# Kernel optimization log

Measured on AMD Instinct MI355X. Metric: run time of the kernel, lower is better.

Reference implementation:

```python
import jax, jax.numpy as jnp
import numpy as np

N = 20000      # nodes
E = 640000     # edges (avg degree 32)
IN = 32        # input_dim
HID = 256      # hidden_dim
H = 8          # num_heads
Dh = HID // H  # head_dim = 32
TD = 32        # time_dim
L = 3          # num_layers
OUT = 2


def setup_inputs() -> dict:
    key = jax.random.key(0)
    ks = jax.random.split(key, 20)
    def w(k, sh):
        return (jax.random.normal(k, sh, jnp.float32) * 0.05)
    return {
        "x": jax.random.normal(ks[0], (N, IN), jnp.float32),
        "timestamps": jax.random.uniform(ks[1], (N,), jnp.float32),
        "edge_index": jax.random.randint(ks[2], (2, E), 0, N, jnp.int32),
        "batch": jnp.zeros((N,), jnp.int32),
        "time_freq": jax.random.normal(ks[3], (TD // 2,), jnp.float32),
        "inW": w(ks[4], (IN, HID)), "inb": jnp.zeros((HID,), jnp.float32),
        "qW": w(ks[5], (L, HID + TD, HID)), "qb": jnp.zeros((L, HID), jnp.float32),
        "kW": w(ks[6], (L, HID + TD, HID)), "kb": jnp.zeros((L, HID), jnp.float32),
        "vW": w(ks[7], (L, HID, HID)), "vb": jnp.zeros((L, HID), jnp.float32),
        "oW": w(ks[8], (L, HID, HID)), "ob": jnp.zeros((L, HID), jnp.float32),
        "c1W": w(ks[9], (HID, HID // 2)), "c1b": jnp.zeros((HID // 2,), jnp.float32),
        "c2W": w(ks[10], (HID // 2, OUT)), "c2b": jnp.zeros((OUT,), jnp.float32),
    }


def reference(x, timestamps, time_freq, inW, inb, qW, qb, kW, kb, vW, vb,
              oW, ob, c1W, c1b, c2W, c2b, edge_index, batch):
    n = x.shape[0]
    src, dst = edge_index[0], edge_index[1]

    # Functional time encoding (node-level timestamps branch)
    t = (timestamps - timestamps.min()) / (timestamps.max() - timestamps.min() + 1e-8)
    wt = t[:, None] * time_freq[None, :]                      # [N, TD/2]
    tf = jnp.concatenate([jnp.cos(wt), jnp.sin(wt)], axis=-1)  # [N, TD]

    h = x @ inW + inb                                          # [N, HID]
    scale = 1.0 / np.sqrt(Dh).astype(np.float32)

    for l in range(L):
        xt = jnp.concatenate([h, tf], axis=-1)                 # [N, HID+TD]
        Q = (xt @ qW[l] + qb[l]).reshape(n, H, Dh)
        K = (xt @ kW[l] + kb[l]).reshape(n, H, Dh)
        V = (h @ vW[l] + vb[l]).reshape(n, H, Dh)

        # per-edge attention scores [E, H]
        scores = jnp.einsum('ehd,ehd->eh', Q[dst], K[src]) * scale

        # segment softmax over incoming edges of each dst node
        m = jax.ops.segment_max(scores, dst, num_segments=n)   # [N, H]
        e = jnp.exp(scores - m[dst])
        s = jax.ops.segment_sum(e, dst, num_segments=n)        # [N, H]
        att = e / s[dst]                                       # [E, H]

        msgs = att[..., None] * V[src]                         # [E, H, Dh]
        out = jax.ops.segment_sum(msgs, dst, num_segments=n)   # [N, H, Dh]
        out = out.reshape(n, HID) @ oW[l] + ob[l]
        h = jax.nn.elu(out)

    # global mean pool (single graph: batch all zeros)
    cnt = jax.ops.segment_sum(jnp.ones((n, 1), h.dtype), batch, num_segments=1)
    g = jax.ops.segment_sum(h, batch, num_segments=1) / jnp.maximum(cnt, 1.0)

    logits = jax.nn.relu(g @ c1W + c1b) @ c2W + c2b            # [1, OUT]
    return logits
```

## Files before the change

### kernel.cpp

```cpp
#include <hip/hip_runtime.h>
#include <math.h>

#define HID 256
#define TD 32
#define NL 3
#define C1DIM 128
#define OUTDIM 2
#define QKVW 768
#define KVSTRIDE 576

using half8  = __attribute__((ext_vector_type(8))) _Float16;
using half4v = __attribute__((ext_vector_type(4))) _Float16;
using half2v = __attribute__((ext_vector_type(2))) _Float16;
using f32x4  = __attribute__((ext_vector_type(4))) float;

typedef __attribute__((address_space(1))) void gbl_void_t;
typedef __attribute__((address_space(3))) void lds_void_t;

__device__ __forceinline__ void load16_to_lds(const void* g, void* l) {
  __builtin_amdgcn_global_load_lds((const gbl_void_t*)g, (lds_void_t*)l, 16, 0, 0);
}

__device__ __forceinline__ int sdot4i(unsigned a, unsigned b, int acc) {
#if __has_builtin(__builtin_amdgcn_sdot4)
  return __builtin_amdgcn_sdot4((int)a, (int)b, acc, false);
#else
#pragma unroll
  for (int i = 0; i < 4; ++i)
    acc += (int)(signed char)(a >> (8 * i)) * (int)(signed char)(b >> (8 * i));
  return acc;
#endif
}

__device__ __forceinline__ void i8x4_to_f32(unsigned w, float* o) {
  o[0] = (float)(int)(signed char)(w);
  o[1] = (float)(int)(signed char)(w >> 8);
  o[2] = (float)(int)(signed char)(w >> 16);
  o[3] = (float)(int)(signed char)(w >> 24);
}

__global__ __launch_bounds__(1024) void k_tsmm(const float* __restrict__ ts,
                                               float* __restrict__ mmf,
                                               int* __restrict__ deg, int n) {
  int t = threadIdx.x;
  float lmin = INFINITY, lmax = -INFINITY;
  for (int i = t; i < n; i += 1024) {
    float v = ts[i];
    lmin = fminf(lmin, v);
    lmax = fmaxf(lmax, v);
    deg[i] = 0;
  }
#pragma unroll
  for (int off = 32; off >= 1; off >>= 1) {
    lmin = fminf(lmin, __shfl_xor(lmin, off));
    lmax = fmaxf(lmax, __shfl_xor(lmax, off));
  }
  __shared__ float wmin[16], wmax[16];
  int lane = t & 63, w = t >> 6;
  if (lane == 0) { wmin[w] = lmin; wmax[w] = lmax; }
  __syncthreads();
  if (t == 0) {
    float a = INFINITY, b = -INFINITY;
    for (int i = 0; i < 16; ++i) { a = fminf(a, wmin[i]); b = fmaxf(b, wmax[i]); }
    mmf[0] = a; mmf[1] = b;
  }
}

__global__ void k_enc(const float* __restrict__ ts, const float* __restrict__ freq,
                      const float* __restrict__ mmf, const float* __restrict__ x,
                      _Float16* __restrict__ tfh, _Float16* __restrict__ xh, int n) {
  int idx = blockIdx.x * blockDim.x + threadIdx.x;
  int nt = n * TD;
  if (idx < nt) {
    int node = idx >> 5, j = idx & 31;
    float t = (ts[node] - mmf[0]) / (mmf[1] - mmf[0] + 1e-8f);
    float w = t * freq[j & 15];
    tfh[idx] = (_Float16)((j < 16) ? cosf(w) : sinf(w));
  } else if (idx < nt + n * 32) {
    int i2 = idx - nt;
    xh[i2] = (_Float16)x[i2];
  }
}

__global__ void k_prep(const float* __restrict__ inW, const float* __restrict__ qW,
                       const float* __restrict__ kW, const float* __restrict__ vW,
                       const float* __restrict__ oW, const float* __restrict__ qb,
                       const float* __restrict__ kb, const float* __restrict__ vb,
                       _Float16* __restrict__ inWt, _Float16* __restrict__ qkvWt,
                       float* __restrict__ qkvb, _Float16* __restrict__ oWt) {
  int idx = blockIdx.x * blockDim.x + threadIdx.x;
  const int S0 = 32 * HID;
  const int KQ = HID + TD;
  const int S1 = NL * QKVW * KQ;
  const int S2 = NL * QKVW;
  const int S3 = NL * HID * HID;
  if (idx < S0) {
    int nrow = idx / 32, k = idx - nrow * 32;
    inWt[idx] = (_Float16)inW[k * HID + nrow];
  } else if ((idx -= S0) < S1) {
    int l = idx / (QKVW * KQ);
    int rem = idx - l * (QKVW * KQ);
    int nrow = rem / KQ;
    int k = rem - nrow * KQ;
    float v;
    if (nrow < 256)      v = qW[(size_t)l * KQ * HID + (size_t)k * HID + nrow];
    else if (nrow < 512) v = kW[(size_t)l * KQ * HID + (size_t)k * HID + (nrow - 256)];
    else                 v = (k < HID) ? vW[(size_t)l * HID * HID + (size_t)k * HID + (nrow - 512)] : 0.f;
    qkvWt[idx] = (_Float16)v;
  } else if ((idx -= S1) < S2) {
    int l = idx / QKVW;
    int j = idx - l * QKVW;
    float v;
    if (j < 256)      v = qb[l * HID + j];
    else if (j < 512) v = kb[l * HID + (j - 256)];
    else              v = vb[l * HID + (j - 512)];
    qkvb[idx] = v;
  } else if ((idx -= S2) < S3) {
    int l = idx / (HID * HID);
    int rem = idx - l * (HID * HID);
    int nrow = rem / HID;
    int k = rem - nrow * HID;
    oWt[idx] = (_Float16)oW[(size_t)l * HID * HID + (size_t)k * HID + nrow];
  }
}

__global__ void k_count(const int* __restrict__ dst, int* deg, int e) {
  int i = blockIdx.x * blockDim.x + threadIdx.x;
  if (i < e) atomicAdd(&deg[dst[i]], 1);
}

__global__ __launch_bounds__(256) void k_scan_part(const int* __restrict__ deg,
                                                   int* __restrict__ bsum, int n) {
  int t = threadIdx.x;
  int idx = blockIdx.x * 256 + t;
  int v = (idx < n) ? deg[idx] : 0;
  int lane = t & 63, w = t >> 6;
  int x = v;
#pragma unroll
  for (int off = 1; off < 64; off <<= 1) {
    int y = __shfl_up(x, off);
    if (lane >= off) x += y;
  }
  __shared__ int ws[4];
  if (lane == 63) ws[w] = x;
  __syncthreads();
  if (t == 0) bsum[blockIdx.x] = ws[0] + ws[1] + ws[2] + ws[3];
}

__global__ __launch_bounds__(64) void k_scan_mid(const int* __restrict__ bsum,
                                                 int* __restrict__ boff, int nb) {
  int lane = threadIdx.x;
  int carry = 0;
  for (int base = 0; base < nb; base += 64) {
    int i = base + lane;
    int v = (i < nb) ? bsum[i] : 0;
    int x = v;
#pragma unroll
    for (int off = 1; off < 64; off <<= 1) {
      int y = __shfl_up(x, off);
      if (lane >= off) x += y;
    }
    if (i < nb) boff[i] = carry + x - v;
    carry += __shfl(x, 63);
  }
}

__global__ __launch_bounds__(256) void k_scan_apply(const int* __restrict__ deg,
                                                    const int* __restrict__ boff,
                                                    int* __restrict__ row_ptr,
                                                    int* __restrict__ cursor, int n, int e) {
  int t = threadIdx.x;
  int idx = blockIdx.x * 256 + t;
  int v = (idx < n) ? deg[idx] : 0;
  int lane = t & 63, w = t >> 6;
  int x = v;
#pragma unroll
  for (int off = 1; off < 64; off <<= 1) {
    int y = __shfl_up(x, off);
    if (lane >= off) x += y;
  }
  __shared__ int ws[4];
  if (lane == 63) ws[w] = x;
  __syncthreads();
  int wpre = 0;
  for (int i = 0; i < w; ++i) wpre += ws[i];
  if (idx < n) {
    row_ptr[idx] = boff[blockIdx.x] + wpre + x - v;
    cursor[idx] = 0;
  }
  if (idx == 0) row_ptr[n] = e;
}

__global__ void k_scatter(const int* __restrict__ src, const int* __restrict__ dst,
                          const int* __restrict__ row_ptr, int* cursor,
                          int* __restrict__ colbuf, int e) {
  int i = blockIdx.x * blockDim.x + threadIdx.x;
  if (i >= e) return;
  int d = dst[i];
  int p = atomicAdd(&cursor[d], 1);
  colbuf[row_ptr[d] + p] = src[i];
}

__global__ __launch_bounds__(256) void k_gemm_f16(
    const _Float16* __restrict__ A1, int K1,
    const _Float16* __restrict__ A2, int K2,
    const _Float16* __restrict__ Bt,
    const float* __restrict__ bias,
    _Float16* __restrict__ C,
    int M, int Ncols, int Ktot, int act) {
  __shared__ half8 smem8[2 * 768];
  char* smem = (char*)smem8;
  const int tid = threadIdx.x;
  const int lane = tid & 63, wave = tid >> 6;
  const int wm = wave >> 1, wn = wave & 1;
  const int row0 = blockIdx.y * 128;
  const int col0 = blockIdx.x * 64;

  auto stage = [&](int buf, int k0) {
    char* sA = smem + buf * 12288;
    char* sB = sA + 8192;
#pragma unroll
    for (int i = 0; i < 2; ++i) {
      int kg = i * 2 + (wave >> 1);
      int row = (wave & 1) * 64 + lane;
      int grow = row0 + row; if (grow > M - 1) grow = M - 1;
      int k = k0 + kg * 8;
      const _Float16* src = (k < K1) ? (A1 + (size_t)grow * K1 + k)
                                     : (A2 + (size_t)grow * K2 + (k - K1));
      load16_to_lds(src, sA + (i * 256 + wave * 64) * 16);
    }
    {
      const _Float16* src = Bt + (size_t)(col0 + lane) * Ktot + k0 + wave * 8;
      load16_to_lds(src, sB + wave * 64 * 16);
    }
  };

  f32x4 acc[4][2];
#pragma unroll
  for (int mf = 0; mf < 4; ++mf)
#pragma unroll
    for (int nf = 0; nf < 2; ++nf) acc[mf][nf] = f32x4{0.f, 0.f, 0.f, 0.f};

  const int nsteps = Ktot >> 5;
  int cur = 0;
  stage(0, 0);
  __syncthreads();
  for (int st = 0; st < nsteps; ++st) {
    if (st + 1 < nsteps) stage(cur ^ 1, (st + 1) * 32);
    char* sA = smem + cur * 12288;
    char* sB = sA + 8192;
    half8 af[4], bf[2];
#pragma unroll
    for (int mf = 0; mf < 4; ++mf) {
      int slot = (lane >> 4) * 128 + wm * 64 + mf * 16 + (lane & 15);
      af[mf] = *(const half8*)(sA + slot * 16);
    }
#pragma unroll
    for (int nf = 0; nf < 2; ++nf) {
      int slot = (lane >> 4) * 64 + wn * 32 + nf * 16 + (lane & 15);
      bf[nf] = *(const half8*)(sB + slot * 16);
    }
#pragma unroll
    for (int mf = 0; mf < 4; ++mf)
#pragma unroll
      for (int nf = 0; nf < 2; ++nf)
        acc[mf][nf] = __builtin_amdgcn_mfma_f32_16x16x32_f16(af[mf], bf[nf], acc[mf][nf], 0, 0, 0);
    __syncthreads();
    cur ^= 1;
  }

  const int rbase = row0 + wm * 64 + (lane >> 4) * 4;
  const int cbase = col0 + wn * 32 + (lane & 15);
#pragma unroll
  for (int nf = 0; nf < 2; ++nf) {
    int col = cbase + nf * 16;
    float bv = bias[col];
#pragma unroll
    for (int mf = 0; mf < 4; ++mf) {
#pragma unroll
      for (int r = 0; r < 4; ++r) {
        int row = rbase + mf * 16 + r;
        if (row < M) {
          float v = acc[mf][nf][r] + bv;
          if (act == 1) v = (v > 0.f) ? v : expm1f(v);
          C[(size_t)row * Ncols + col] = (_Float16)v;
        }
      }
    }
  }
}

__global__ __launch_bounds__(256) void k_cvt8(const _Float16* __restrict__ QKV,
                                              unsigned char* __restrict__ KV8, int n) {
  int node = blockIdx.x * 8 + (threadIdx.x >> 5);
  if (node >= n) return;
  int t32 = threadIdx.x & 31;
  const _Float16* base = QKV + (size_t)node * QKVW + t32 * 8;
  half8 kh = *(const half8*)(base + 256);
  half8 vh = *(const half8*)(base + 512);
  float kf[8], vf[8];
  float kmax = 0.f, vmax = 0.f;
#pragma unroll
  for (int j = 0; j < 8; ++j) {
    kf[j] = (float)kh[j]; kmax = fmaxf(kmax, fabsf(kf[j]));
    vf[j] = (float)vh[j]; vmax = fmaxf(vmax, fabsf(vf[j]));
  }
  kmax = fmaxf(kmax, __shfl_xor(kmax, 1)); kmax = fmaxf(kmax, __shfl_xor(kmax, 2));
  vmax = fmaxf(vmax, __shfl_xor(vmax, 1)); vmax = fmaxf(vmax, __shfl_xor(vmax, 2));
  float kinv = (kmax > 0.f) ? (127.f / kmax) : 0.f;
  float vinv = (vmax > 0.f) ? (127.f / vmax) : 0.f;
  unsigned kp0 = 0, kp1 = 0, vp0 = 0, vp1 = 0;
#pragma unroll
  for (int j = 0; j < 4; ++j) {
    kp0 |= ((unsigned)((int)rintf(kf[j] * kinv)) & 255u) << (8 * j);
    kp1 |= ((unsigned)((int)rintf(kf[j + 4] * kinv)) & 255u) << (8 * j);
    vp0 |= ((unsigned)((int)rintf(vf[j] * vinv)) & 255u) << (8 * j);
    vp1 |= ((unsigned)((int)rintf(vf[j + 4] * vinv)) & 255u) << (8 * j);
  }
  unsigned char* out = KV8 + (size_t)node * KVSTRIDE;
  *(uint2*)(out + t32 * 8) = uint2{kp0, kp1};
  *(uint2*)(out + 256 + t32 * 8) = uint2{vp0, vp1};
  if ((t32 & 3) == 0) {
    half2v sp;
    sp.x = (_Float16)(kmax * (1.f / 127.f));
    sp.y = (_Float16)(vmax * (1.f / 127.f));
    *(half2v*)(out + 512 + (t32 >> 2) * 4) = sp;
  }
}

__global__ __launch_bounds__(256) void k_attn(const _Float16* __restrict__ QKV,
                                              const unsigned char* __restrict__ KV8,
                                              const int* __restrict__ row_ptr,
                                              const int* __restrict__ colbuf,
                                              _Float16* __restrict__ out, int n) {
  __shared__ float sm_m[4][8], sm_s[4][8];
  __shared__ float sm_a[4][32][9];
  int tid = threadIdx.x;
  int g = tid >> 5, t32 = tid & 31;
  int nl = g >> 1, hf = g & 1;
  int node = blockIdx.x * 4 + nl;
  bool act = node < n;
  int beg = 0, end = 0;
  if (act) { beg = row_ptr[node]; end = row_ptr[node + 1]; }
  int mid = beg + ((end - beg + 1) >> 1);
  int lo = hf ? mid : beg;
  int hi = hf ? end : mid;
  int d = t32 * 8;
  const float scale = 0.17677669529663687f;

  float qf[8] = {0.f, 0.f, 0.f, 0.f, 0.f, 0.f, 0.f, 0.f};
  if (act) {
    half8 qh = *(const half8*)(QKV + (size_t)node * QKVW + d);
#pragma unroll
    for (int j = 0; j < 8; ++j) qf[j] = (float)qh[j] * scale;
  }
  float qmax = 0.f;
#pragma unroll
  for (int j = 0; j < 8; ++j) qmax = fmaxf(qmax, fabsf(qf[j]));
  qmax = fmaxf(qmax, __shfl_xor(qmax, 1));
  qmax = fmaxf(qmax, __shfl_xor(qmax, 2));
  float qinv = (qmax > 0.f) ? (127.f / qmax) : 0.f;
  float sq = qmax * (1.f / 127.f);
  unsigned q8x = 0, q8y = 0;
#pragma unroll
  for (int j = 0; j < 4; ++j) {
    q8x |= ((unsigned)((int)rintf(qf[j] * qinv)) & 255u) << (8 * j);
    q8y |= ((unsigned)((int)rintf(qf[j + 4] * qinv)) & 255u) << (8 * j);
  }

  float m = -INFINITY, s = 0.f;
  float a[8] = {0.f, 0.f, 0.f, 0.f, 0.f, 0.f, 0.f, 0.f};
  int scoff = 512 + (t32 >> 2) * 4;

  for (int i = lo; i < hi; i += 4) {
    uint2 kb[4], vb[4];
    float skj[4], svj[4];
#pragma unroll
    for (int j = 0; j < 4; ++j) {
      int ii = i + j; if (ii > hi - 1) ii = hi - 1;
      int sn = colbuf[ii];
      const unsigned char* b = KV8 + (size_t)sn * KVSTRIDE;
      kb[j] = *(const uint2*)(b + t32 * 8);
      vb[j] = *(const uint2*)(b + 256 + t32 * 8);
      unsigned scw = *(const unsigned*)(b + scoff);
      union { unsigned u; half2v h; } sc; sc.u = scw;
      skj[j] = (float)sc.h.x;
      svj[j] = (float)sc.h.y;
    }
    float p[4];
#pragma unroll
    for (int j = 0; j < 4; ++j) {
      int idot = sdot4i(kb[j].x, q8x, 0);
      idot = sdot4i(kb[j].y, q8y, idot);
      p[j] = (float)idot;
    }
#pragma unroll
    for (int j = 0; j < 4; ++j) {
      p[j] += __shfl_xor(p[j], 1);
      p[j] += __shfl_xor(p[j], 2);
      p[j] *= sq * skj[j];
      if (i + j >= hi) p[j] = -INFINITY;
    }
#pragma unroll
    for (int j = 0; j < 4; ++j) {
      float vf[8];
      i8x4_to_f32(vb[j].x, vf);
      i8x4_to_f32(vb[j].y, vf + 4);
      float sc_ = p[j];
      if (sc_ <= m) {
        float e2 = __expf(sc_ - m);
        s += e2;
        float ev = e2 * svj[j];
#pragma unroll
        for (int q = 0; q < 8; ++q) a[q] = fmaf(ev, vf[q], a[q]);
      } else {
        float f = __expf(m - sc_);
        s = s * f + 1.f;
#pragma unroll
        for (int q = 0; q < 8; ++q) a[q] = fmaf(a[q], f, svj[j] * vf[q]);
        m = sc_;
      }
    }
  }

  if (hf == 1 && act) {
    if ((t32 & 3) == 0) { sm_m[nl][t32 >> 2] = m; sm_s[nl][t32 >> 2] = s; }
#pragma unroll
    for (int q = 0; q < 8; ++q) sm_a[nl][t32][q] = a[q];
  }
  __syncthreads();
  if (hf == 0 && act) {
    float m1 = sm_m[nl][t32 >> 2], s1 = sm_s[nl][t32 >> 2];
    float M = fmaxf(m, m1);
    float f0 = (s > 0.f) ? __expf(m - M) : 0.f;
    float f1 = (s1 > 0.f) ? __expf(m1 - M) : 0.f;
    float S = s * f0 + s1 * f1;
    float inv = (S > 0.f) ? (1.f / S) : 0.f;
    half8 o;
#pragma unroll
    for (int q = 0; q < 8; ++q) o[q] = (_Float16)((a[q] * f0 + sm_a[nl][t32][q] * f1) * inv);
    *(half8*)(out + (size_t)node * HID + d) = o;
  }
}

__global__ __launch_bounds__(256) void k_pool_partial(const _Float16* __restrict__ h,
                                                      float* __restrict__ partial, int n) {
  int b = blockIdx.x, t = threadIdx.x;
  float s = 0.f;
  for (int r = b; r < n; r += 256) s += (float)h[(size_t)r * HID + t];
  partial[b * HID + t] = s;
}

__global__ __launch_bounds__(256) void k_final(const float* __restrict__ partial,
                                               const float* __restrict__ c1W,
                                               const float* __restrict__ c1b,
                                               const float* __restrict__ c2W,
                                               const float* __restrict__ c2b,
                                               float* __restrict__ out, int n) {
  __shared__ float gl[HID];
  __shared__ float r1[C1DIM];
  int t = threadIdx.x;
  float s = 0.f;
  for (int b = 0; b < 256; b++) s += partial[b * HID + t];
  gl[t] = s / (float)n;
  __syncthreads();
  if (t < C1DIM) {
    float a = c1b[t];
    for (int k = 0; k < HID; k++) a += gl[k] * c1W[k * C1DIM + t];
    r1[t] = fmaxf(a, 0.f);
  }
  __syncthreads();
  if (t < OUTDIM) {
    float a = c2b[t];
    for (int k = 0; k < C1DIM; k++) a += r1[k] * c2W[k * OUTDIM + t];
    out[t] = a;
  }
}

extern "C" void kernel_launch(void* const* d_in, const int* in_sizes, int n_in,
                              void* d_out, int out_size, void* d_ws, size_t ws_size,
                              hipStream_t stream) {
  const float* x    = (const float*)d_in[0];
  const float* ts   = (const float*)d_in[1];
  const int*   ei   = (const int*)d_in[2];
  const float* freq = (const float*)d_in[4];
  const float* inW  = (const float*)d_in[5];
  const float* inb  = (const float*)d_in[6];
  const float* qW   = (const float*)d_in[7];
  const float* qb   = (const float*)d_in[8];
  const float* kW   = (const float*)d_in[9];
  const float* kb   = (const float*)d_in[10];
  const float* vW   = (const float*)d_in[11];
  const float* vb   = (const float*)d_in[12];
  const float* oW   = (const float*)d_in[13];
  const float* ob   = (const float*)d_in[14];
  const float* c1W  = (const float*)d_in[15];
  const float* c1b  = (const float*)d_in[16];
  const float* c2W  = (const float*)d_in[17];
  const float* c2b  = (const float*)d_in[18];

  int n = in_sizes[1];
  int e = in_sizes[2] / 2;
  const int* src = ei;
  const int* dst = ei + e;
  int nb = (n + 255) / 256;

  char* w = (char*)d_ws;
  size_t off = 0;
  auto alloc = [&](size_t bytes) -> char* {
    char* p = w + off;
    off = (off + bytes + 255) & ~(size_t)255;
    return p;
  };
  _Float16* tfh     = (_Float16*)alloc((size_t)n * TD * 2);
  _Float16* xh      = (_Float16*)alloc((size_t)n * 32 * 2);
  _Float16* h       = (_Float16*)alloc((size_t)n * HID * 2);
  _Float16* QKV     = (_Float16*)alloc((size_t)n * QKVW * 2);
  unsigned char* KV8 = (unsigned char*)alloc((size_t)n * KVSTRIDE);
  _Float16* ao      = (_Float16*)alloc((size_t)n * HID * 2);
  _Float16* inWt    = (_Float16*)alloc((size_t)32 * HID * 2);
  _Float16* qkvWt   = (_Float16*)alloc((size_t)NL * QKVW * (HID + TD) * 2);
  float*    qkvb    = (float*)alloc((size_t)NL * QKVW * 4);
  _Float16* oWt     = (_Float16*)alloc((size_t)NL * HID * HID * 2);
  int*      deg     = (int*)alloc((size_t)n * 4);
  int*      cursor  = (int*)alloc((size_t)n * 4);
  int*      row_ptr = (int*)alloc((size_t)(n + 1) * 4);
  int*      colbuf  = (int*)alloc((size_t)e * 4);
  int*      bsum    = (int*)alloc((size_t)nb * 4);
  int*      boff    = (int*)alloc((size_t)nb * 4);
  float*    partial = (float*)alloc((size_t)256 * HID * 4);
  float*    mmf     = (float*)alloc(256);

  int b256 = 256;
  hipLaunchKernelGGL(k_tsmm, dim3(1), dim3(1024), 0, stream, ts, mmf, deg, n);
  hipLaunchKernelGGL(k_enc, dim3((n * 64 + 255) / 256), dim3(b256), 0, stream,
                     ts, freq, mmf, x, tfh, xh, n);
  {
    int total = 32 * HID + NL * QKVW * (HID + TD) + NL * QKVW + NL * HID * HID;
    hipLaunchKernelGGL(k_prep, dim3((total + 255) / 256), dim3(b256), 0, stream,
                       inW, qW, kW, vW, oW, qb, kb, vb, inWt, qkvWt, qkvb, oWt);
  }
  hipLaunchKernelGGL(k_count, dim3((e + 255) / 256), dim3(b256), 0, stream, dst, deg, e);
  hipLaunchKernelGGL(k_scan_part, dim3(nb), dim3(b256), 0, stream, deg, bsum, n);
  hipLaunchKernelGGL(k_scan_mid, dim3(1), dim3(64), 0, stream, bsum, boff, nb);
  hipLaunchKernelGGL(k_scan_apply, dim3(nb), dim3(b256), 0, stream, deg, boff, row_ptr, cursor, n, e);
  hipLaunchKernelGGL(k_scatter, dim3((e + 255) / 256), dim3(b256), 0, stream, src, dst, row_ptr, cursor, colbuf, e);

  dim3 ggrid_h(HID / 64, (n + 127) / 128);
  dim3 ggrid_qkv(QKVW / 64, (n + 127) / 128);
  hipLaunchKernelGGL(k_gemm_f16, ggrid_h, dim3(b256), 0, stream,
                     xh, 32, xh, 32, inWt, inb, h, n, HID, 32, 0);

  for (int l = 0; l < NL; ++l) {
    const _Float16* qkvWtl = qkvWt + (size_t)l * QKVW * (HID + TD);
    const float*    qkvbl  = qkvb + (size_t)l * QKVW;
    const _Float16* oWtl   = oWt + (size_t)l * HID * HID;
    hipLaunchKernelGGL(k_gemm_f16, ggrid_qkv, dim3(b256), 0, stream,
                       h, HID, tfh, TD, qkvWtl, qkvbl, QKV, n, QKVW, HID + TD, 0);
    hipLaunchKernelGGL(k_cvt8, dim3((n + 7) / 8), dim3(b256), 0, stream,
                       QKV, KV8, n);
    hipLaunchKernelGGL(k_attn, dim3((n + 3) / 4), dim3(b256), 0, stream,
                       QKV, KV8, row_ptr, colbuf, ao, n);
    hipLaunchKernelGGL(k_gemm_f16, ggrid_h, dim3(b256), 0, stream,
                       ao, HID, ao, HID, oWtl, ob + l * HID, h, n, HID, HID, 1);
  }

  hipLaunchKernelGGL(k_pool_partial, dim3(256), dim3(b256), 0, stream, h, partial, n);
  hipLaunchKernelGGL(k_final, dim3(1), dim3(b256), 0, stream, partial, c1W, c1b, c2W, c2b, (float*)d_out, n);
}
```

Baseline: 480.4 us.

## Store int8 K/V head-major and assign one 8-lane group per node-head in attention

The quantized K/V buffer changes from node-major to head-major: each head of each node gets a 64-byte row with K and V bytes interleaved, and the per-head scales move to a separate array. The attention kernel now has each block handle one head for 32 nodes, with 8 lanes per node-head walking the whole edge list. This removes the two-way edge split and its shared-memory merge, and keeps each block's gathers inside one head's slice so they stay local in cache. In exchange, each node's edge list is processed serially per head, so nodes with many edges run longer with no split to spread the work, and the dot-product reduction needs an extra shuffle step.

```diff
diff --git a/kernel.cpp b/kernel.cpp
--- a/kernel.cpp
+++ b/kernel.cpp
@@ -7,7 +7,6 @@
 #define C1DIM 128
 #define OUTDIM 2
 #define QKVW 768
-#define KVSTRIDE 576
 
 using half8  = __attribute__((ext_vector_type(8))) _Float16;
 using half4v = __attribute__((ext_vector_type(4))) _Float16;
@@ -30,13 +29,6 @@
     acc += (int)(signed char)(a >> (8 * i)) * (int)(signed char)(b >> (8 * i));
   return acc;
 #endif
-}
-
-__device__ __forceinline__ void i8x4_to_f32(unsigned w, float* o) {
-  o[0] = (float)(int)(signed char)(w);
-  o[1] = (float)(int)(signed char)(w >> 8);
-  o[2] = (float)(int)(signed char)(w >> 16);
-  o[3] = (float)(int)(signed char)(w >> 24);
 }
 
 __global__ __launch_bounds__(1024) void k_tsmm(const float* __restrict__ ts,
@@ -291,10 +283,12 @@
 }
 
 __global__ __launch_bounds__(256) void k_cvt8(const _Float16* __restrict__ QKV,
-                                              unsigned char* __restrict__ KV8, int n) {
+                                              unsigned char* __restrict__ KV8,
+                                              half2v* __restrict__ SC, int n) {
   int node = blockIdx.x * 8 + (threadIdx.x >> 5);
   if (node >= n) return;
   int t32 = threadIdx.x & 31;
+  int h = t32 >> 2, p = t32 & 3;
   const _Float16* base = QKV + (size_t)node * QKVW + t32 * 8;
   half8 kh = *(const half8*)(base + 256);
   half8 vh = *(const half8*)(base + 512);
@@ -317,130 +311,104 @@
     vp0 |= ((unsigned)((int)rintf(vf[j] * vinv)) & 255u) << (8 * j);
     vp1 |= ((unsigned)((int)rintf(vf[j + 4] * vinv)) & 255u) << (8 * j);
   }
-  unsigned char* out = KV8 + (size_t)node * KVSTRIDE;
-  *(uint2*)(out + t32 * 8) = uint2{kp0, kp1};
-  *(uint2*)(out + 256 + t32 * 8) = uint2{vp0, vp1};
-  if ((t32 & 3) == 0) {
+  unsigned char* out = KV8 + (((size_t)h * n + node) << 6);
+  *(uint2*)(out + (2 * p) * 8)     = uint2{kp0, vp0};
+  *(uint2*)(out + (2 * p + 1) * 8) = uint2{kp1, vp1};
+  if (p == 0) {
     half2v sp;
     sp.x = (_Float16)(kmax * (1.f / 127.f));
     sp.y = (_Float16)(vmax * (1.f / 127.f));
-    *(half2v*)(out + 512 + (t32 >> 2) * 4) = sp;
+    SC[(size_t)h * n + node] = sp;
   }
 }
 
 __global__ __launch_bounds__(256) void k_attn(const _Float16* __restrict__ QKV,
                                               const unsigned char* __restrict__ KV8,
+                                              const half2v* __restrict__ SC,
                                               const int* __restrict__ row_ptr,
                                               const int* __restrict__ colbuf,
                                               _Float16* __restrict__ out, int n) {
-  __shared__ float sm_m[4][8], sm_s[4][8];
-  __shared__ float sm_a[4][32][9];
-  int tid = threadIdx.x;
-  int g = tid >> 5, t32 = tid & 31;
-  int nl = g >> 1, hf = g & 1;
-  int node = blockIdx.x * 4 + nl;
-  bool act = node < n;
-  int beg = 0, end = 0;
-  if (act) { beg = row_ptr[node]; end = row_ptr[node + 1]; }
-  int mid = beg + ((end - beg + 1) >> 1);
-  int lo = hf ? mid : beg;
-  int hi = hf ? end : mid;
-  int d = t32 * 8;
+  int h = blockIdx.x & 7;
+  int node = (blockIdx.x >> 3) * 32 + (threadIdx.x >> 3);
+  if (node >= n) return;
+  int j = threadIdx.x & 7;
   const float scale = 0.17677669529663687f;
-
-  float qf[8] = {0.f, 0.f, 0.f, 0.f, 0.f, 0.f, 0.f, 0.f};
-  if (act) {
-    half8 qh = *(const half8*)(QKV + (size_t)node * QKVW + d);
-#pragma unroll
-    for (int j = 0; j < 8; ++j) qf[j] = (float)qh[j] * scale;
-  }
-  float qmax = 0.f;
-#pragma unroll
-  for (int j = 0; j < 8; ++j) qmax = fmaxf(qmax, fabsf(qf[j]));
+  const unsigned char* KVh = KV8 + (((size_t)h * n) << 6);
+  const half2v* SCh = SC + (size_t)h * n;
+
+  half4v qh = *(const half4v*)(QKV + (size_t)node * QKVW + h * 32 + j * 4);
+  float qf[4];
+#pragma unroll
+  for (int q = 0; q < 4; ++q) qf[q] = (float)qh[q] * scale;
+  float qmax = fmaxf(fmaxf(fabsf(qf[0]), fabsf(qf[1])), fmaxf(fabsf(qf[2]), fabsf(qf[3])));
   qmax = fmaxf(qmax, __shfl_xor(qmax, 1));
   qmax = fmaxf(qmax, __shfl_xor(qmax, 2));
+  qmax = fmaxf(qmax, __shfl_xor(qmax, 4));
   float qinv = (qmax > 0.f) ? (127.f / qmax) : 0.f;
   float sq = qmax * (1.f / 127.f);
-  unsigned q8x = 0, q8y = 0;
-#pragma unroll
-  for (int j = 0; j < 4; ++j) {
-    q8x |= ((unsigned)((int)rintf(qf[j] * qinv)) & 255u) << (8 * j);
-    q8y |= ((unsigned)((int)rintf(qf[j + 4] * qinv)) & 255u) << (8 * j);
-  }
-
+  unsigned q8 = 0;
+#pragma unroll
+  for (int q = 0; q < 4; ++q)
+    q8 |= ((unsigned)((int)rintf(qf[q] * qinv)) & 255u) << (8 * q);
+
+  int beg = row_ptr[node], end = row_ptr[node + 1];
   float m = -INFINITY, s = 0.f;
-  float a[8] = {0.f, 0.f, 0.f, 0.f, 0.f, 0.f, 0.f, 0.f};
-  int scoff = 512 + (t32 >> 2) * 4;
-
-  for (int i = lo; i < hi; i += 4) {
-    uint2 kb[4], vb[4];
-    float skj[4], svj[4];
-#pragma unroll
-    for (int j = 0; j < 4; ++j) {
-      int ii = i + j; if (ii > hi - 1) ii = hi - 1;
+  float a[4] = {0.f, 0.f, 0.f, 0.f};
+
+  for (int i = beg; i < end; i += 4) {
+    uint2 kv[4];
+    float sk[4], sv[4];
+#pragma unroll
+    for (int t = 0; t < 4; ++t) {
+      int ii = i + t; if (ii > end - 1) ii = end - 1;
       int sn = colbuf[ii];
-      const unsigned char* b = KV8 + (size_t)sn * KVSTRIDE;
-      kb[j] = *(const uint2*)(b + t32 * 8);
-      vb[j] = *(const uint2*)(b + 256 + t32 * 8);
-      unsigned scw = *(const unsigned*)(b + scoff);
-      union { unsigned u; half2v h; } sc; sc.u = scw;
-      skj[j] = (float)sc.h.x;
-      svj[j] = (float)sc.h.y;
+      kv[t] = *(const uint2*)(KVh + ((size_t)sn << 6) + j * 8);
+      half2v sc = SCh[sn];
+      sk[t] = (float)sc.x;
+      sv[t] = (float)sc.y;
     }
     float p[4];
 #pragma unroll
-    for (int j = 0; j < 4; ++j) {
-      int idot = sdot4i(kb[j].x, q8x, 0);
-      idot = sdot4i(kb[j].y, q8y, idot);
-      p[j] = (float)idot;
-    }
-#pragma unroll
-    for (int j = 0; j < 4; ++j) {
-      p[j] += __shfl_xor(p[j], 1);
-      p[j] += __shfl_xor(p[j], 2);
-      p[j] *= sq * skj[j];
-      if (i + j >= hi) p[j] = -INFINITY;
-    }
-#pragma unroll
-    for (int j = 0; j < 4; ++j) {
-      float vf[8];
-      i8x4_to_f32(vb[j].x, vf);
-      i8x4_to_f32(vb[j].y, vf + 4);
-      float sc_ = p[j];
+    for (int t = 0; t < 4; ++t) {
+      int idot = sdot4i(kv[t].x, q8, 0);
+      float pf = (float)idot;
+      pf += __shfl_xor(pf, 1);
+      pf += __shfl_xor(pf, 2);
+      pf += __shfl_xor(pf, 4);
+      pf *= sq * sk[t];
+      if (i + t >= end) pf = -INFINITY;
+      p[t] = pf;
+    }
+#pragma unroll
+    for (int t = 0; t < 4; ++t) {
+      float vf[4];
+      vf[0] = (float)(int)(signed char)(kv[t].y);
+      vf[1] = (float)(int)(signed char)(kv[t].y >> 8);
+      vf[2] = (float)(int)(signed char)(kv[t].y >> 16);
+      vf[3] = (float)(int)(signed char)(kv[t].y >> 24);
+      float sc_ = p[t];
       if (sc_ <= m) {
         float e2 = __expf(sc_ - m);
         s += e2;
-        float ev = e2 * svj[j];
-#pragma unroll
-        for (int q = 0; q < 8; ++q) a[q] = fmaf(ev, vf[q], a[q]);
+        float ev = e2 * sv[t];
+#pragma unroll
+        for (int q = 0; q < 4; ++q) a[q] = fmaf(ev, vf[q], a[q]);
       } else {
         float f = __expf(m - sc_);
         s = s * f + 1.f;
-#pragma unroll
-        for (int q = 0; q < 8; ++q) a[q] = fmaf(a[q], f, svj[j] * vf[q]);
+        float ev = sv[t];
+#pragma unroll
+        for (int q = 0; q < 4; ++q) a[q] = fmaf(a[q], f, ev * vf[q]);
         m = sc_;
       }
     }
   }
 
-  if (hf == 1 && act) {
-    if ((t32 & 3) == 0) { sm_m[nl][t32 >> 2] = m; sm_s[nl][t32 >> 2] = s; }
-#pragma unroll
-    for (int q = 0; q < 8; ++q) sm_a[nl][t32][q] = a[q];
-  }
-  __syncthreads();
-  if (hf == 0 && act) {
-    float m1 = sm_m[nl][t32 >> 2], s1 = sm_s[nl][t32 >> 2];
-    float M = fmaxf(m, m1);
-    float f0 = (s > 0.f) ? __expf(m - M) : 0.f;
-    float f1 = (s1 > 0.f) ? __expf(m1 - M) : 0.f;
-    float S = s * f0 + s1 * f1;
-    float inv = (S > 0.f) ? (1.f / S) : 0.f;
-    half8 o;
-#pragma unroll
-    for (int q = 0; q < 8; ++q) o[q] = (_Float16)((a[q] * f0 + sm_a[nl][t32][q] * f1) * inv);
-    *(half8*)(out + (size_t)node * HID + d) = o;
-  }
+  float inv = (s > 0.f) ? (1.f / s) : 0.f;
+  half4v o;
+#pragma unroll
+  for (int q = 0; q < 4; ++q) o[q] = (_Float16)(a[q] * inv);
+  *(half4v*)(out + (size_t)node * HID + h * 32 + j * 4) = o;
 }
 
 __global__ __launch_bounds__(256) void k_pool_partial(const _Float16* __restrict__ h,
@@ -516,7 +484,8 @@
   _Float16* xh      = (_Float16*)alloc((size_t)n * 32 * 2);
   _Float16* h       = (_Float16*)alloc((size_t)n * HID * 2);
   _Float16* QKV     = (_Float16*)alloc((size_t)n * QKVW * 2);
-  unsigned char* KV8 = (unsigned char*)alloc((size_t)n * KVSTRIDE);
+  unsigned char* KV8 = (unsigned char*)alloc((size_t)n * 512);
+  half2v*   SC      = (half2v*)alloc((size_t)n * 8 * 4);
   _Float16* ao      = (_Float16*)alloc((size_t)n * HID * 2);
   _Float16* inWt    = (_Float16*)alloc((size_t)32 * HID * 2);
   _Float16* qkvWt   = (_Float16*)alloc((size_t)NL * QKVW * (HID + TD) * 2);
@@ -551,6 +520,7 @@
   hipLaunchKernelGGL(k_gemm_f16, ggrid_h, dim3(b256), 0, stream,
                      xh, 32, xh, 32, inWt, inb, h, n, HID, 32, 0);
 
+  int nchunks = (n + 31) / 32;
   for (int l = 0; l < NL; ++l) {
     const _Float16* qkvWtl = qkvWt + (size_t)l * QKVW * (HID + TD);
     const float*    qkvbl  = qkvb + (size_t)l * QKVW;
@@ -558,9 +528,9 @@
     hipLaunchKernelGGL(k_gemm_f16, ggrid_qkv, dim3(b256), 0, stream,
                        h, HID, tfh, TD, qkvWtl, qkvbl, QKV, n, QKVW, HID + TD, 0);
     hipLaunchKernelGGL(k_cvt8, dim3((n + 7) / 8), dim3(b256), 0, stream,
-                       QKV, KV8, n);
-    hipLaunchKernelGGL(k_attn, dim3((n + 3) / 4), dim3(b256), 0, stream,
-                       QKV, KV8, row_ptr, colbuf, ao, n);
+                       QKV, KV8, SC, n);
+    hipLaunchKernelGGL(k_attn, dim3(nchunks * 8), dim3(b256), 0, stream,
+                       QKV, KV8, SC, row_ptr, colbuf, ao, n);
     hipLaunchKernelGGL(k_gemm_f16, ggrid_h, dim3(b256), 0, stream,
                        ao, HID, ao, HID, oWtl, ob + l * HID, h, n, HID, HID, 1);
   }
```

Result: slower. 519.4 us (+8.1%).
